# Kernel tuning notes

Hardware: AMD Instinct MI355X
Metric: run time of the kernel (lower is better)

The kernel has to match this reference:

```python
import jax, jax.numpy as jnp
import numpy as np

OUTPUT_SIZE = 50000
HIDDEN = 512


def setup_inputs() -> dict:
    key = jax.random.key(0)
    k1, k2, k3, k4 = jax.random.split(key, 4)
    input_value = jax.random.normal(k1, (4, 2048, HIDDEN), dtype=jnp.float32)
    mask_tensor = jax.random.randint(k2, (4, 2048, 32), 0, OUTPUT_SIZE, dtype=jnp.int64)
    weight = jax.random.normal(k3, (OUTPUT_SIZE, HIDDEN), dtype=jnp.float32)
    bias = jax.random.uniform(k4, (OUTPUT_SIZE,), dtype=jnp.float32)
    return {"input_value": input_value, "mask_tensor": mask_tensor,
            "weight": weight, "bias": bias}


def reference(input_value, mask_tensor, weight, bias):
    # gather per-token candidate weights: [b, s, m, h]
    part_weight = weight[mask_tensor]
    # gather per-token candidate biases: [b, s, m]
    part_bias = bias[mask_tensor]
    out = jnp.einsum('bsh,bsmh->bsm', input_value, part_weight) + part_bias
    return jax.nn.relu(out)
```

## Files before the change

kernel.cpp:

```cpp
#include <hip/hip_runtime.h>
#include <hip/hip_bf16.h>

#define HIDDEN 512
#define M_PER_TOKEN 32
#define BUCKET_CAP 32

typedef _Float16 half8 __attribute__((ext_vector_type(8)));
typedef float    f32x4 __attribute__((ext_vector_type(4)));

__global__ __launch_bounds__(256) void prep_kernel(
    const float* __restrict__ input,
    _Float16*    __restrict__ in_h,
    int*         __restrict__ counts,
    int*         __restrict__ padded,
    int n_chunks, int n_rows)
{
    int i = blockIdx.x * 256 + threadIdx.x;
    if (i < n_chunks) {
        const float4 a = ((const float4*)input)[2 * i];
        const float4 b = ((const float4*)input)[2 * i + 1];
        half8 h;
        h[0] = (_Float16)a.x; h[1] = (_Float16)a.y;
        h[2] = (_Float16)a.z; h[3] = (_Float16)a.w;
        h[4] = (_Float16)b.x; h[5] = (_Float16)b.y;
        h[6] = (_Float16)b.z; h[7] = (_Float16)b.w;
        ((half8*)in_h)[i] = h;
    }
    if (i < n_rows) {
        counts[i] = 0;
        *(int4*)(padded + ((size_t)i << 5)) = make_int4(0, 0, 0, 0);
    }
}

__global__ __launch_bounds__(256) void scatter_kernel(
    const int* __restrict__ mask,
    int*       __restrict__ counts,
    int*       __restrict__ padded,
    int n_pairs)
{
    int i = blockIdx.x * 256 + threadIdx.x;
    if (i >= n_pairs) return;
    int r = mask[i];
    int slot = atomicAdd(&counts[r], 1);
    if (slot < BUCKET_CAP) padded[(r << 5) + slot] = i;
}

template <int CTRL>
__device__ __forceinline__ float dpp_add(float v) {
    return v + __int_as_float(__builtin_amdgcn_update_dpp(
        0, __float_as_int(v), CTRL, 0xF, 0xF, true));
}

__device__ __forceinline__ float red16(float v) {
    v = dpp_add<0xB1>(v);
    v = dpp_add<0x4E>(v);
    v = dpp_add<0x141>(v);
    v = dpp_add<0x140>(v);
    return v;
}

__device__ __forceinline__ float dot128(const half8 h, const f32x4 wa,
                                        const f32x4 wb) {
    return (float)h[0]*wa[0] + (float)h[1]*wa[1]
         + (float)h[2]*wa[2] + (float)h[3]*wa[3]
         + (float)h[4]*wb[0] + (float)h[5]*wb[1]
         + (float)h[6]*wb[2] + (float)h[7]*wb[3];
}

__global__ __launch_bounds__(256) void row_ffn_kernel(
    const _Float16* __restrict__ in_h,
    const float*    __restrict__ weight,
    const float*    __restrict__ bias,
    const int*      __restrict__ counts,
    const int*      __restrict__ padded,
    float*          __restrict__ out,
    int n_rows, int blocks_per_xcd)
{
    const int b    = (int)blockIdx.x;
    const int bsw  = (b & 7) * blocks_per_xcd + (b >> 3);
    const int wave = threadIdx.x >> 6;
    const int lane = threadIdx.x & 63;
    const int s    = lane & 15;
    const int q    = lane >> 4;
    const int r    = bsw * 4 + wave;
    if (r >= n_rows) return;

    const int* users = padded + ((size_t)r << 5);

    const int   c_raw = counts[r];
    const int   pid0  = users[q];
    const float bv    = bias[r];

    const float* wbase = weight + (size_t)r * HIDDEN + s * 8;
    f32x4 w[8];
#pragma unroll
    for (int j = 0; j < 4; ++j) {
        w[2*j]   = __builtin_nontemporal_load((const f32x4*)(wbase + j*128));
        w[2*j+1] = __builtin_nontemporal_load((const f32x4*)(wbase + j*128 + 4));
    }

    const _Float16* irow0 = in_h + (size_t)(pid0 >> 5) * HIDDEN + s * 8;
    const half8 h0 = *(const half8*)(irow0);
    const half8 h1 = *(const half8*)(irow0 + 128);
    const half8 h2 = *(const half8*)(irow0 + 256);
    const half8 h3 = *(const half8*)(irow0 + 384);

    const int c = (c_raw > BUCKET_CAP) ? BUCKET_CAP : c_raw;

    int pid_n = 0;
    if (c > 4) {
        const int g4  = c - 4;
        const int off = (q < g4) ? q : (g4 - 1);
        pid_n = users[4 + off];
    }

    float d = dot128(h0, w[0], w[1]) + dot128(h1, w[2], w[3])
            + dot128(h2, w[4], w[5]) + dot128(h3, w[6], w[7]);
    d = red16(d);
    if (s == 0 && q < c) {
        float v = d + bv;
        out[pid0] = v > 0.0f ? v : 0.0f;
    }

    for (int u = 4; u < c; u += 4) {
        const int g   = c - u;
        const int pid = pid_n;

        const _Float16* irow = in_h + (size_t)(pid >> 5) * HIDDEN + s * 8;
        const half8 g0 = *(const half8*)(irow);
        const half8 g1 = *(const half8*)(irow + 128);
        const half8 g2 = *(const half8*)(irow + 256);
        const half8 g3 = *(const half8*)(irow + 384);

        if (u + 4 < c) {
            const int gn  = c - (u + 4);
            const int off = (q < gn) ? q : (gn - 1);
            pid_n = users[u + 4 + off];
        }

        float e = dot128(g0, w[0], w[1]) + dot128(g1, w[2], w[3])
                + dot128(g2, w[4], w[5]) + dot128(g3, w[6], w[7]);
        e = red16(e);
        if (s == 0 && q < g) {
            float v = e + bv;
            out[pid] = v > 0.0f ? v : 0.0f;
        }
    }
}

__global__ __launch_bounds__(256) void dynamic_ffn_f32_kernel(
    const float* __restrict__ input,
    const int*   __restrict__ mask,
    const float* __restrict__ weight,
    const float* __restrict__ bias,
    float*       __restrict__ out,
    int n_tokens)
{
    const int token = blockIdx.x;
    if (token >= n_tokens) return;
    const int wave = threadIdx.x >> 6;
    const int lane = threadIdx.x & 63;

    const float* in_row = input + (size_t)token * HIDDEN + lane * 8;
    const float4 x0 = *(const float4*)(in_row);
    const float4 x1 = *(const float4*)(in_row + 4);

    const int* midx = mask + (size_t)token * M_PER_TOKEN + wave * 8;
    float*     orow = out  + (size_t)token * M_PER_TOKEN + wave * 8;

    int idx[8];
#pragma unroll
    for (int j = 0; j < 8; ++j) idx[j] = midx[j];

    float acc[8];
#pragma unroll
    for (int j = 0; j < 8; ++j) {
        const float* w = weight + (size_t)idx[j] * HIDDEN + lane * 8;
        const float4 a = *(const float4*)(w);
        const float4 b = *(const float4*)(w + 4);
        acc[j] = x0.x * a.x + x0.y * a.y + x0.z * a.z + x0.w * a.w
               + x1.x * b.x + x1.y * b.y + x1.z * b.z + x1.w * b.w;
    }
#pragma unroll
    for (int j = 0; j < 8; ++j) {
        float p = acc[j];
#pragma unroll
        for (int off = 32; off > 0; off >>= 1)
            p += __shfl_down(p, off, 64);
        if (lane == 0) {
            float v = p + bias[idx[j]];
            orow[j] = v > 0.0f ? v : 0.0f;
        }
    }
}

extern "C" void kernel_launch(void* const* d_in, const int* in_sizes, int n_in,
                              void* d_out, int out_size, void* d_ws, size_t ws_size,
                              hipStream_t stream) {
    const float* input  = (const float*)d_in[0];
    const int*   mask   = (const int*)  d_in[1];
    const float* weight = (const float*)d_in[2];
    const float* bias   = (const float*)d_in[3];
    float*       out    = (float*)d_out;

    const int n_tokens = in_sizes[0] / HIDDEN;
    const int n_pairs  = in_sizes[1];
    const int n_rows   = in_sizes[2] / HIDDEN;

    const size_t in_h_bytes   = (size_t)in_sizes[0] * sizeof(_Float16);
    const size_t counts_bytes = (size_t)n_rows * sizeof(int);
    const size_t padded_bytes = (size_t)n_rows * BUCKET_CAP * sizeof(int);
    const size_t need = in_h_bytes + counts_bytes + padded_bytes;

    if (ws_size >= need) {
        _Float16* in_h   = (_Float16*)d_ws;
        int*      counts = (int*)((char*)d_ws + in_h_bytes);
        int*      padded = (int*)((char*)d_ws + in_h_bytes + counts_bytes);

        const int n_chunks = in_sizes[0] / 8;
        prep_kernel<<<(n_chunks + 255) / 256, 256, 0, stream>>>(
            input, in_h, counts, padded, n_chunks, n_rows);

        scatter_kernel<<<(n_pairs + 255) / 256, 256, 0, stream>>>(
            mask, counts, padded, n_pairs);

        const int n_wave_rows    = (n_rows + 3) / 4;
        const int blocks_per_xcd = (n_wave_rows + 7) / 8;
        const int grid           = blocks_per_xcd * 8;
        row_ffn_kernel<<<grid, 256, 0, stream>>>(
            in_h, weight, bias, counts, padded, out, n_rows, blocks_per_xcd);
    } else {
        dynamic_ffn_f32_kernel<<<n_tokens, 256, 0, stream>>>(
            input, mask, weight, bias, out, n_tokens);
    }
}
```

Baseline: 202.6 us.

## Fuse prep and scatter kernels and map four weight rows per wave

```diff
diff --git a/kernel.cpp b/kernel.cpp
--- a/kernel.cpp
+++ b/kernel.cpp
@@ -8,41 +8,49 @@
 typedef _Float16 half8 __attribute__((ext_vector_type(8)));
 typedef float    f32x4 __attribute__((ext_vector_type(4)));
 
-__global__ __launch_bounds__(256) void prep_kernel(
+__global__ __launch_bounds__(256) void prep_scatter_kernel(
     const float* __restrict__ input,
     _Float16*    __restrict__ in_h,
+    const int*   __restrict__ mask,
     int*         __restrict__ counts,
     int*         __restrict__ padded,
-    int n_chunks, int n_rows)
+    int n_chunks, int n_pairs, int conv_blocks)
 {
-    int i = blockIdx.x * 256 + threadIdx.x;
-    if (i < n_chunks) {
-        const float4 a = ((const float4*)input)[2 * i];
-        const float4 b = ((const float4*)input)[2 * i + 1];
-        half8 h;
-        h[0] = (_Float16)a.x; h[1] = (_Float16)a.y;
-        h[2] = (_Float16)a.z; h[3] = (_Float16)a.w;
-        h[4] = (_Float16)b.x; h[5] = (_Float16)b.y;
-        h[6] = (_Float16)b.z; h[7] = (_Float16)b.w;
-        ((half8*)in_h)[i] = h;
-    }
-    if (i < n_rows) {
-        counts[i] = 0;
-        *(int4*)(padded + ((size_t)i << 5)) = make_int4(0, 0, 0, 0);
-    }
-}
-
-__global__ __launch_bounds__(256) void scatter_kernel(
-    const int* __restrict__ mask,
-    int*       __restrict__ counts,
-    int*       __restrict__ padded,
-    int n_pairs)
-{
-    int i = blockIdx.x * 256 + threadIdx.x;
-    if (i >= n_pairs) return;
-    int r = mask[i];
-    int slot = atomicAdd(&counts[r], 1);
-    if (slot < BUCKET_CAP) padded[(r << 5) + slot] = i;
+    const int bid = blockIdx.x;
+    if (bid < conv_blocks) {
+        int i = bid * 256 + threadIdx.x;
+        if (i < n_chunks) {
+            const float4 a = ((const float4*)input)[2 * i];
+            const float4 b = ((const float4*)input)[2 * i + 1];
+            half8 h;
+            h[0] = (_Float16)a.x; h[1] = (_Float16)a.y;
+            h[2] = (_Float16)a.z; h[3] = (_Float16)a.w;
+            h[4] = (_Float16)b.x; h[5] = (_Float16)b.y;
+            h[6] = (_Float16)b.z; h[7] = (_Float16)b.w;
+            ((half8*)in_h)[i] = h;
+        }
+    } else {
+        int t    = (bid - conv_blocks) * 256 + threadIdx.x;
+        int base = t * 4;
+        if (base + 3 < n_pairs) {
+            const int4 m = *(const int4*)(mask + base);
+            int r, slot;
+            r = m.x; slot = atomicAdd(&counts[r], 1);
+            if (slot < BUCKET_CAP) padded[(r << 5) + slot] = base;
+            r = m.y; slot = atomicAdd(&counts[r], 1);
+            if (slot < BUCKET_CAP) padded[(r << 5) + slot] = base + 1;
+            r = m.z; slot = atomicAdd(&counts[r], 1);
+            if (slot < BUCKET_CAP) padded[(r << 5) + slot] = base + 2;
+            r = m.w; slot = atomicAdd(&counts[r], 1);
+            if (slot < BUCKET_CAP) padded[(r << 5) + slot] = base + 3;
+        } else {
+            for (int i = base; i < n_pairs; ++i) {
+                int r = mask[i];
+                int slot = atomicAdd(&counts[r], 1);
+                if (slot < BUCKET_CAP) padded[(r << 5) + slot] = i;
+            }
+        }
+    }
 }
 
 template <int CTRL>
@@ -74,7 +82,7 @@
     const int*      __restrict__ counts,
     const int*      __restrict__ padded,
     float*          __restrict__ out,
-    int n_rows, int blocks_per_xcd)
+    int n_rows, int n_pairs, int blocks_per_xcd)
 {
     const int b    = (int)blockIdx.x;
     const int bsw  = (b & 7) * blocks_per_xcd + (b >> 3);
@@ -82,69 +90,53 @@
     const int lane = threadIdx.x & 63;
     const int s    = lane & 15;
     const int q    = lane >> 4;
-    const int r    = bsw * 4 + wave;
-    if (r >= n_rows) return;
-
-    const int* users = padded + ((size_t)r << 5);
-
-    const int   c_raw = counts[r];
-    const int   pid0  = users[q];
-    const float bv    = bias[r];
-
-    const float* wbase = weight + (size_t)r * HIDDEN + s * 8;
-    f32x4 w[8];
-#pragma unroll
-    for (int j = 0; j < 4; ++j) {
-        w[2*j]   = __builtin_nontemporal_load((const f32x4*)(wbase + j*128));
-        w[2*j+1] = __builtin_nontemporal_load((const f32x4*)(wbase + j*128 + 4));
-    }
-
-    const _Float16* irow0 = in_h + (size_t)(pid0 >> 5) * HIDDEN + s * 8;
-    const half8 h0 = *(const half8*)(irow0);
-    const half8 h1 = *(const half8*)(irow0 + 128);
-    const half8 h2 = *(const half8*)(irow0 + 256);
-    const half8 h3 = *(const half8*)(irow0 + 384);
-
-    const int c = (c_raw > BUCKET_CAP) ? BUCKET_CAP : c_raw;
-
-    int pid_n = 0;
-    if (c > 4) {
-        const int g4  = c - 4;
-        const int off = (q < g4) ? q : (g4 - 1);
-        pid_n = users[4 + off];
-    }
-
-    float d = dot128(h0, w[0], w[1]) + dot128(h1, w[2], w[3])
-            + dot128(h2, w[4], w[5]) + dot128(h3, w[6], w[7]);
-    d = red16(d);
-    if (s == 0 && q < c) {
-        float v = d + bv;
-        out[pid0] = v > 0.0f ? v : 0.0f;
-    }
-
-    for (int u = 4; u < c; u += 4) {
-        const int g   = c - u;
-        const int pid = pid_n;
-
-        const _Float16* irow = in_h + (size_t)(pid >> 5) * HIDDEN + s * 8;
-        const half8 g0 = *(const half8*)(irow);
-        const half8 g1 = *(const half8*)(irow + 128);
-        const half8 g2 = *(const half8*)(irow + 256);
-        const half8 g3 = *(const half8*)(irow + 384);
-
-        if (u + 4 < c) {
-            const int gn  = c - (u + 4);
-            const int off = (q < gn) ? q : (gn - 1);
-            pid_n = users[u + 4 + off];
-        }
-
-        float e = dot128(g0, w[0], w[1]) + dot128(g1, w[2], w[3])
-                + dot128(g2, w[4], w[5]) + dot128(g3, w[6], w[7]);
-        e = red16(e);
-        if (s == 0 && q < g) {
-            float v = e + bv;
-            out[pid] = v > 0.0f ? v : 0.0f;
-        }
+
+    const int r = bsw * 16 + wave * 4 + q;
+    if (bsw * 16 >= n_rows) return;
+    const int rc = (r < n_rows) ? r : n_rows - 1;
+
+    const int* users = padded + ((size_t)rc << 5);
+
+    const int   c_raw = counts[rc];
+    int         pid   = users[0];
+    const float bv    = bias[rc];
+
+    const float* wbase = weight + (size_t)rc * HIDDEN + s * 8;
+    const f32x4 w0 = __builtin_nontemporal_load((const f32x4*)(wbase +   0));
+    const f32x4 w1 = __builtin_nontemporal_load((const f32x4*)(wbase +   4));
+    const f32x4 w2 = __builtin_nontemporal_load((const f32x4*)(wbase + 128));
+    const f32x4 w3 = __builtin_nontemporal_load((const f32x4*)(wbase + 132));
+    const f32x4 w4 = __builtin_nontemporal_load((const f32x4*)(wbase + 256));
+    const f32x4 w5 = __builtin_nontemporal_load((const f32x4*)(wbase + 260));
+    const f32x4 w6 = __builtin_nontemporal_load((const f32x4*)(wbase + 384));
+    const f32x4 w7 = __builtin_nontemporal_load((const f32x4*)(wbase + 388));
+
+    int c = (r < n_rows) ? ((c_raw > BUCKET_CAP) ? BUCKET_CAP : c_raw) : 0;
+    if ((unsigned)pid >= (unsigned)n_pairs) pid = 0;
+
+    for (int i = 0; ; ++i) {
+        const bool act = i < c;
+        if (__ballot(act) == 0ull) break;
+
+        int pidn = users[(i + 1) & 31];
+        if ((unsigned)pidn >= (unsigned)n_pairs) pidn = 0;
+
+        if (act) {
+            const _Float16* ir = in_h + (size_t)(pid >> 5) * HIDDEN + s * 8;
+            const half8 h0 = *(const half8*)(ir);
+            const half8 h1 = *(const half8*)(ir + 128);
+            const half8 h2 = *(const half8*)(ir + 256);
+            const half8 h3 = *(const half8*)(ir + 384);
+
+            float d = dot128(h0, w0, w1) + dot128(h1, w2, w3)
+                    + dot128(h2, w4, w5) + dot128(h3, w6, w7);
+            d = red16(d);
+            if (s == 0) {
+                float v = d + bv;
+                out[pid] = v > 0.0f ? v : 0.0f;
+            }
+        }
+        pid = pidn;
     }
 }
 
@@ -217,18 +209,21 @@
         int*      counts = (int*)((char*)d_ws + in_h_bytes);
         int*      padded = (int*)((char*)d_ws + in_h_bytes + counts_bytes);
 
-        const int n_chunks = in_sizes[0] / 8;
-        prep_kernel<<<(n_chunks + 255) / 256, 256, 0, stream>>>(
-            input, in_h, counts, padded, n_chunks, n_rows);
-
-        scatter_kernel<<<(n_pairs + 255) / 256, 256, 0, stream>>>(
-            mask, counts, padded, n_pairs);
-
-        const int n_wave_rows    = (n_rows + 3) / 4;
-        const int blocks_per_xcd = (n_wave_rows + 7) / 8;
+        hipMemsetAsync(counts, 0, counts_bytes, stream);
+
+        const int n_chunks    = in_sizes[0] / 8;
+        const int conv_blocks = (n_chunks + 255) / 256;
+        const int sc_threads  = (n_pairs + 3) / 4;
+        const int sc_blocks   = (sc_threads + 255) / 256;
+        prep_scatter_kernel<<<conv_blocks + sc_blocks, 256, 0, stream>>>(
+            input, in_h, mask, counts, padded, n_chunks, n_pairs, conv_blocks);
+
+        const int n_blocks       = (n_rows + 15) / 16;
+        const int blocks_per_xcd = (n_blocks + 7) / 8;
         const int grid           = blocks_per_xcd * 8;
         row_ffn_kernel<<<grid, 256, 0, stream>>>(
-            in_h, weight, bias, counts, padded, out, n_rows, blocks_per_xcd);
+            in_h, weight, bias, counts, padded, out,
+            n_rows, n_pairs, blocks_per_xcd);
     } else {
         dynamic_ffn_f32_kernel<<<n_tokens, 256, 0, stream>>>(
             input, mask, weight, bias, out, n_tokens);
```

Result: slower. 210.1 us (+3.7%).
